# Performance work log

Hardware: AMD Instinct MI355X
Metric: run time of the kernel (lower is better)

The kernel has to match this reference:

```python
import jax, jax.numpy as jnp
import numpy as np

D_K = 64
EPS = 1e-6


def setup_inputs() -> dict:
    key = jax.random.key(0)
    ks = jax.random.split(key, 6)
    B, S, D2, DV = 4, 2048, 1024, 64
    q = jax.random.normal(ks[0], (B, S, D2), dtype=jnp.float32)
    k = jax.random.normal(ks[1], (B, S, D2), dtype=jnp.float32)
    v = jax.random.normal(ks[2], (B, S, D2), dtype=jnp.float32)
    mask = jax.random.randint(ks[3], (B, S, S), 0, 2) == 1
    V = jax.random.normal(ks[4], (1, DV), dtype=jnp.float32)
    fc_w = jax.random.normal(ks[5], (D2, DV), dtype=jnp.float32) * (1.0 / np.sqrt(DV))
    fc_b = jnp.zeros((D2,), dtype=jnp.float32)
    ln_g = jnp.ones((D2,), dtype=jnp.float32)
    ln_b = jnp.zeros((D2,), dtype=jnp.float32)
    return {"q": q, "k": k, "v": v, "mask": mask, "V": V,
            "fc_w": fc_w, "fc_b": fc_b, "ln_g": ln_g, "ln_b": ln_b}


def _layer_norm(x, g, b):
    mu = jnp.mean(x, axis=-1, keepdims=True)
    var = jnp.var(x, axis=-1, keepdims=True)
    return (x - mu) * jax.lax.rsqrt(var + EPS) * g + b


def reference(q, k, v, mask, V, fc_w, fc_b, ln_g, ln_b):
    residual = q
    qn = _layer_norm(q, ln_g, ln_b)
    # scaled dot-product scores (no softmax in this variant)
    attn = jnp.einsum('bsd,btd->bst', qn / jnp.sqrt(jnp.float32(D_K)), k)
    attn = jnp.where(mask, 0.0, attn)  # masked_fill with 0
    # v_ = V broadcast over (batch, seq, key); attn @ v_ == row-sum outer V
    output = jnp.sum(attn, axis=-1, keepdims=True) * V  # [B,S,d_v]
    output = output @ fc_w.T + fc_b                     # [B,S,2*d_model]
    output = output + residual
    return (output, attn)
```

## Files before the change

kernel.cpp:

```cpp
#include <hip/hip_runtime.h>
#include <hip/hip_bf16.h>
#include <cstdint>

#define S_LEN 2048
#define D2_   1024
#define DV_   64
#define NB_   4

typedef __bf16 bf16x8 __attribute__((ext_vector_type(8)));
typedef float  f32x4  __attribute__((ext_vector_type(4)));

__device__ __forceinline__ unsigned short f2bf(float f) {
  union { float f; unsigned int u; } v; v.f = f;
  unsigned int r = v.u + 0x7fffu + ((v.u >> 16) & 1u);
  return (unsigned short)(r >> 16);
}

__device__ __forceinline__ void async16(const unsigned short* g, unsigned short* l) {
  __builtin_amdgcn_global_load_lds(
      (__attribute__((address_space(1))) void*)g,
      (__attribute__((address_space(3))) void*)l,
      16, 0, 0);
}

__global__ void __launch_bounds__(256) prep_kernel(
    const float* __restrict__ q, const float* __restrict__ k,
    const float* __restrict__ gam, const float* __restrict__ bet,
    const float* __restrict__ V, const float* __restrict__ fw,
    unsigned short* __restrict__ qn, unsigned short* __restrict__ kb,
    float* __restrict__ w2) {
  const int row = blockIdx.x;
  const int t = threadIdx.x;

  const float4 x = ((const float4*)(q + (size_t)row * D2_))[t];
  float s  = x.x + x.y + x.z + x.w;
  float ss = x.x * x.x + x.y * x.y + x.z * x.z + x.w * x.w;
  #pragma unroll
  for (int o = 32; o > 0; o >>= 1) { s += __shfl_down(s, o); ss += __shfl_down(ss, o); }
  __shared__ float red[8];
  if ((t & 63) == 0) { red[t >> 6] = s; red[(t >> 6) + 4] = ss; }
  __syncthreads();
  const float tot  = red[0] + red[1] + red[2] + red[3];
  const float tots = red[4] + red[5] + red[6] + red[7];
  const float mu  = tot * (1.0f / D2_);
  const float var = tots * (1.0f / D2_) - mu * mu;
  const float rs  = rsqrtf(var + 1e-6f) * 0.125f;
  const float4 gv = ((const float4*)gam)[t];
  const float4 bv = ((const float4*)bet)[t];
  ushort4 o4;
  o4.x = f2bf((x.x - mu) * rs * gv.x + 0.125f * bv.x);
  o4.y = f2bf((x.y - mu) * rs * gv.y + 0.125f * bv.y);
  o4.z = f2bf((x.z - mu) * rs * gv.z + 0.125f * bv.z);
  o4.w = f2bf((x.w - mu) * rs * gv.w + 0.125f * bv.w);
  ((ushort4*)(qn + (size_t)row * D2_))[t] = o4;

  const float4 kx = ((const float4*)(k + (size_t)row * D2_))[t];
  ushort4 k4;
  k4.x = f2bf(kx.x); k4.y = f2bf(kx.y); k4.z = f2bf(kx.z); k4.w = f2bf(kx.w);
  ((ushort4*)(kb + (size_t)row * D2_))[t] = k4;

  if (row < 4) {
    const int d = row * 256 + t;
    const float4* r  = (const float4*)(fw + (size_t)d * DV_);
    const float4* vv = (const float4*)V;
    float acc = 0.f;
    #pragma unroll
    for (int j = 0; j < 16; ++j) {
      const float4 a = r[j], b = vv[j];
      acc += a.x * b.x + a.y * b.y + a.z * b.z + a.w * b.w;
    }
    w2[d] = acc;
  }
}

__global__ void __launch_bounds__(256) attn_gemm_kernel(
    const unsigned short* __restrict__ qn,
    const unsigned short* __restrict__ kb,
    const int* __restrict__ mask,
    float* __restrict__ attn) {
  __shared__ __align__(16) unsigned short Asm_[2][128 * 32];
  __shared__ __align__(16) unsigned short Bsm_[2][128 * 32];

  const int t  = threadIdx.x;
  const int bn = blockIdx.x * 128;
  const int bm = blockIdx.y * 128;
  const int bt = blockIdx.z;

  const unsigned short* gA = qn + ((size_t)bt * S_LEN + bm + (t >> 2)) * D2_ + (t & 3) * 8;
  const unsigned short* gB = kb + ((size_t)bt * S_LEN + bn + (t >> 2)) * D2_ + (t & 3) * 8;

  const int lane = t & 63;
  const int w  = t >> 6;
  const int wm = (w >> 1) * 64;
  const int wn = (w & 1) * 64;
  const int lr = lane & 15;
  const int lg = lane >> 4;

  f32x4 acc[4][4] = {};

  async16(gA, Asm_[0] + t * 8);
  async16(gA + 64 * D2_, Asm_[0] + t * 8 + 2048);
  async16(gB, Bsm_[0] + t * 8);
  async16(gB + 64 * D2_, Bsm_[0] + t * 8 + 2048);
  gA += 32; gB += 32;

  #pragma unroll 4
  for (int it = 0; it < 32; ++it) {
    __syncthreads();
    const unsigned short* Ac = Asm_[it & 1];
    const unsigned short* Bc = Bsm_[it & 1];
    if (it < 31) {
      unsigned short* An = Asm_[(it + 1) & 1];
      unsigned short* Bn = Bsm_[(it + 1) & 1];
      async16(gA, An + t * 8);
      async16(gA + 64 * D2_, An + t * 8 + 2048);
      async16(gB, Bn + t * 8);
      async16(gB + 64 * D2_, Bn + t * 8 + 2048);
      gA += 32; gB += 32;
    }
    bf16x8 af[4], bfv[4];
    #pragma unroll
    for (int f = 0; f < 4; ++f) {
      af[f]  = *(const bf16x8*)(Ac + (wm + f * 16 + lr) * 32 + lg * 8);
      bfv[f] = *(const bf16x8*)(Bc + (wn + f * 16 + lr) * 32 + lg * 8);
    }
    #pragma unroll
    for (int fm = 0; fm < 4; ++fm)
      #pragma unroll
      for (int fn = 0; fn < 4; ++fn)
        acc[fm][fn] = __builtin_amdgcn_mfma_f32_16x16x32_bf16(
            af[fm], bfv[fn], acc[fm][fn], 0, 0, 0);
  }

  #pragma unroll
  for (int fm = 0; fm < 4; ++fm) {
    #pragma unroll
    for (int r = 0; r < 4; ++r) {
      const int srow = bm + wm + fm * 16 + lg * 4 + r;
      const size_t off = ((size_t)bt * S_LEN + srow) * S_LEN + bn + wn;
      const int* mrow = mask + off;
      float*    arow = attn + off;
      #pragma unroll
      for (int fn = 0; fn < 4; ++fn) {
        const int c = fn * 16 + lr;
        float vv = acc[fm][fn][r];
        vv = mrow[c] ? 0.0f : vv;
        arow[c] = vv;
      }
    }
  }
}

__global__ void __launch_bounds__(256) out_kernel(
    const float* __restrict__ attn, const float* __restrict__ q,
    const float* __restrict__ w2, const float* __restrict__ fcb,
    float* __restrict__ out) {
  const int row = blockIdx.x;
  const int t = threadIdx.x;
  const float4* ar = (const float4*)(attn + (size_t)row * S_LEN);
  const float4 a = ar[t], b = ar[t + 256];
  float s = a.x + a.y + a.z + a.w + b.x + b.y + b.z + b.w;
  #pragma unroll
  for (int o = 32; o > 0; o >>= 1) s += __shfl_down(s, o);
  __shared__ float red[4];
  if ((t & 63) == 0) red[t >> 6] = s;
  __syncthreads();
  const float rs = red[0] + red[1] + red[2] + red[3];
  const float4 wv = ((const float4*)w2)[t];
  const float4 bv = ((const float4*)fcb)[t];
  const float4 qv = ((const float4*)(q + (size_t)row * D2_))[t];
  float4 o4;
  o4.x = rs * wv.x + bv.x + qv.x;
  o4.y = rs * wv.y + bv.y + qv.y;
  o4.z = rs * wv.z + bv.z + qv.z;
  o4.w = rs * wv.w + bv.w + qv.w;
  ((float4*)(out + (size_t)row * D2_))[t] = o4;
}

extern "C" void kernel_launch(void* const* d_in, const int* in_sizes, int n_in,
                              void* d_out, int out_size, void* d_ws, size_t ws_size,
                              hipStream_t stream) {
  (void)in_sizes; (void)n_in; (void)out_size; (void)ws_size;
  const float* q    = (const float*)d_in[0];
  const float* k    = (const float*)d_in[1];
  const int*   mask = (const int*)d_in[3];
  const float* V    = (const float*)d_in[4];
  const float* fw   = (const float*)d_in[5];
  const float* fcb  = (const float*)d_in[6];
  const float* lg   = (const float*)d_in[7];
  const float* lb   = (const float*)d_in[8];

  float* out  = (float*)d_out;
  float* attn = out + (size_t)NB_ * S_LEN * D2_;

  unsigned short* qn = (unsigned short*)out;
  unsigned short* kb = qn + (size_t)NB_ * S_LEN * D2_;
  float* w2 = (float*)d_ws;

  prep_kernel<<<NB_ * S_LEN, 256, 0, stream>>>(q, k, lg, lb, V, fw, qn, kb, w2);
  attn_gemm_kernel<<<dim3(S_LEN / 128, S_LEN / 128, NB_), 256, 0, stream>>>(qn, kb, mask, attn);
  out_kernel<<<NB_ * S_LEN, 256, 0, stream>>>(attn, q, w2, fcb, out);
}
```

Baseline: 295.6 us.

## Fuse row-sum into GEMM epilogue with atomics, switch to 32x32 MFMA and swizzled LDS

```diff
diff --git a/kernel.cpp b/kernel.cpp
--- a/kernel.cpp
+++ b/kernel.cpp
@@ -8,7 +8,7 @@
 #define NB_   4
 
 typedef __bf16 bf16x8 __attribute__((ext_vector_type(8)));
-typedef float  f32x4  __attribute__((ext_vector_type(4)));
+typedef float  f32x16 __attribute__((ext_vector_type(16)));
 
 __device__ __forceinline__ unsigned short f2bf(float f) {
   union { float f; unsigned int u; } v; v.f = f;
@@ -28,9 +28,11 @@
     const float* __restrict__ gam, const float* __restrict__ bet,
     const float* __restrict__ V, const float* __restrict__ fw,
     unsigned short* __restrict__ qn, unsigned short* __restrict__ kb,
-    float* __restrict__ w2) {
+    float* __restrict__ w2, float* __restrict__ rowsum) {
   const int row = blockIdx.x;
   const int t = threadIdx.x;
+
+  if (row < 32) rowsum[row * 256 + t] = 0.0f;
 
   const float4 x = ((const float4*)(q + (size_t)row * D2_))[t];
   float s  = x.x + x.y + x.z + x.w;
@@ -77,95 +79,91 @@
     const unsigned short* __restrict__ qn,
     const unsigned short* __restrict__ kb,
     const int* __restrict__ mask,
-    float* __restrict__ attn) {
-  __shared__ __align__(16) unsigned short Asm_[2][128 * 32];
-  __shared__ __align__(16) unsigned short Bsm_[2][128 * 32];
+    float* __restrict__ attn,
+    float* __restrict__ rowsum) {
+  __shared__ __align__(16) unsigned short Asm_[128 * 32];
+  __shared__ __align__(16) unsigned short Bsm_[128 * 32];
 
   const int t  = threadIdx.x;
   const int bn = blockIdx.x * 128;
   const int bm = blockIdx.y * 128;
   const int bt = blockIdx.z;
 
-  const unsigned short* gA = qn + ((size_t)bt * S_LEN + bm + (t >> 2)) * D2_ + (t & 3) * 8;
-  const unsigned short* gB = kb + ((size_t)bt * S_LEN + bn + (t >> 2)) * D2_ + (t & 3) * 8;
+  const int srow_ = t >> 2;
+  const int kg_   = (t & 3) ^ (srow_ & 3);
+  const unsigned short* gA = qn + ((size_t)bt * S_LEN + bm + srow_) * D2_ + kg_ * 8;
+  const unsigned short* gB = kb + ((size_t)bt * S_LEN + bn + srow_) * D2_ + kg_ * 8;
+  unsigned short* lA = Asm_ + t * 8;
+  unsigned short* lB = Bsm_ + t * 8;
 
   const int lane = t & 63;
-  const int w  = t >> 6;
-  const int wm = (w >> 1) * 64;
-  const int wn = (w & 1) * 64;
-  const int lr = lane & 15;
-  const int lg = lane >> 4;
-
-  f32x4 acc[4][4] = {};
-
-  async16(gA, Asm_[0] + t * 8);
-  async16(gA + 64 * D2_, Asm_[0] + t * 8 + 2048);
-  async16(gB, Bsm_[0] + t * 8);
-  async16(gB + 64 * D2_, Bsm_[0] + t * 8 + 2048);
-  gA += 32; gB += 32;
-
-  #pragma unroll 4
-  for (int it = 0; it < 32; ++it) {
+  const int w    = t >> 6;
+  const int wm   = (w >> 1) * 64;
+  const int wn   = (w & 1) * 64;
+  const int col  = lane & 31;
+  const int half = lane >> 5;
+
+  const int x0 = (half ^ (lane & 3)) * 8;
+  const int x1 = ((2 + half) ^ (lane & 3)) * 8;
+
+  f32x16 acc[2][2] = {};
+
+  for (int k0 = 0; k0 < D2_; k0 += 32) {
+    async16(gA, lA);
+    async16(gA + 64 * D2_, lA + 2048);
+    async16(gB, lB);
+    async16(gB + 64 * D2_, lB + 2048);
+    gA += 32; gB += 32;
     __syncthreads();
-    const unsigned short* Ac = Asm_[it & 1];
-    const unsigned short* Bc = Bsm_[it & 1];
-    if (it < 31) {
-      unsigned short* An = Asm_[(it + 1) & 1];
-      unsigned short* Bn = Bsm_[(it + 1) & 1];
-      async16(gA, An + t * 8);
-      async16(gA + 64 * D2_, An + t * 8 + 2048);
-      async16(gB, Bn + t * 8);
-      async16(gB + 64 * D2_, Bn + t * 8 + 2048);
-      gA += 32; gB += 32;
+
+    bf16x8 af[2][2], bfv[2][2];
+    #pragma unroll
+    for (int f = 0; f < 2; ++f) {
+      const int ra = (wm + f * 32 + col) * 32;
+      const int rb = (wn + f * 32 + col) * 32;
+      af[f][0]  = *(const bf16x8*)(Asm_ + ra + x0);
+      af[f][1]  = *(const bf16x8*)(Asm_ + ra + x1);
+      bfv[f][0] = *(const bf16x8*)(Bsm_ + rb + x0);
+      bfv[f][1] = *(const bf16x8*)(Bsm_ + rb + x1);
     }
-    bf16x8 af[4], bfv[4];
-    #pragma unroll
-    for (int f = 0; f < 4; ++f) {
-      af[f]  = *(const bf16x8*)(Ac + (wm + f * 16 + lr) * 32 + lg * 8);
-      bfv[f] = *(const bf16x8*)(Bc + (wn + f * 16 + lr) * 32 + lg * 8);
-    }
-    #pragma unroll
-    for (int fm = 0; fm < 4; ++fm)
+    #pragma unroll
+    for (int s = 0; s < 2; ++s)
       #pragma unroll
-      for (int fn = 0; fn < 4; ++fn)
-        acc[fm][fn] = __builtin_amdgcn_mfma_f32_16x16x32_bf16(
-            af[fm], bfv[fn], acc[fm][fn], 0, 0, 0);
+      for (int fm = 0; fm < 2; ++fm)
+        #pragma unroll
+        for (int fn = 0; fn < 2; ++fn)
+          acc[fm][fn] = __builtin_amdgcn_mfma_f32_32x32x16_bf16(
+              af[fm][s], bfv[fn][s], acc[fm][fn], 0, 0, 0);
+    __syncthreads();
   }
 
   #pragma unroll
-  for (int fm = 0; fm < 4; ++fm) {
-    #pragma unroll
-    for (int r = 0; r < 4; ++r) {
-      const int srow = bm + wm + fm * 16 + lg * 4 + r;
-      const size_t off = ((size_t)bt * S_LEN + srow) * S_LEN + bn + wn;
-      const int* mrow = mask + off;
-      float*    arow = attn + off;
+  for (int fm = 0; fm < 2; ++fm) {
+    #pragma unroll
+    for (int r = 0; r < 16; ++r) {
+      const int srow = bm + wm + fm * 32 + (r & 3) + 8 * (r >> 2) + 4 * half;
+      const size_t base = ((size_t)bt * S_LEN + srow) * S_LEN + bn + wn;
+      float v0 = acc[fm][0][r];
+      float v1 = acc[fm][1][r];
+      v0 = mask[base + col] ? 0.0f : v0;
+      v1 = mask[base + 32 + col] ? 0.0f : v1;
+      attn[base + col]      = v0;
+      attn[base + 32 + col] = v1;
+      float s = v0 + v1;
       #pragma unroll
-      for (int fn = 0; fn < 4; ++fn) {
-        const int c = fn * 16 + lr;
-        float vv = acc[fm][fn][r];
-        vv = mrow[c] ? 0.0f : vv;
-        arow[c] = vv;
-      }
+      for (int o = 16; o > 0; o >>= 1) s += __shfl_down(s, o, 32);
+      if (col == 0) atomicAdd(rowsum + (size_t)bt * S_LEN + srow, s);
     }
   }
 }
 
 __global__ void __launch_bounds__(256) out_kernel(
-    const float* __restrict__ attn, const float* __restrict__ q,
+    const float* __restrict__ rowsum, const float* __restrict__ q,
     const float* __restrict__ w2, const float* __restrict__ fcb,
     float* __restrict__ out) {
   const int row = blockIdx.x;
   const int t = threadIdx.x;
-  const float4* ar = (const float4*)(attn + (size_t)row * S_LEN);
-  const float4 a = ar[t], b = ar[t + 256];
-  float s = a.x + a.y + a.z + a.w + b.x + b.y + b.z + b.w;
-  #pragma unroll
-  for (int o = 32; o > 0; o >>= 1) s += __shfl_down(s, o);
-  __shared__ float red[4];
-  if ((t & 63) == 0) red[t >> 6] = s;
-  __syncthreads();
-  const float rs = red[0] + red[1] + red[2] + red[3];
+  const float rs = rowsum[row];
   const float4 wv = ((const float4*)w2)[t];
   const float4 bv = ((const float4*)fcb)[t];
   const float4 qv = ((const float4*)(q + (size_t)row * D2_))[t];
@@ -195,9 +193,10 @@
 
   unsigned short* qn = (unsigned short*)out;
   unsigned short* kb = qn + (size_t)NB_ * S_LEN * D2_;
-  float* w2 = (float*)d_ws;
-
-  prep_kernel<<<NB_ * S_LEN, 256, 0, stream>>>(q, k, lg, lb, V, fw, qn, kb, w2);
-  attn_gemm_kernel<<<dim3(S_LEN / 128, S_LEN / 128, NB_), 256, 0, stream>>>(qn, kb, mask, attn);
-  out_kernel<<<NB_ * S_LEN, 256, 0, stream>>>(attn, q, w2, fcb, out);
-}
+  float* w2     = (float*)d_ws;
+  float* rowsum = w2 + D2_;
+
+  prep_kernel<<<NB_ * S_LEN, 256, 0, stream>>>(q, k, lg, lb, V, fw, qn, kb, w2, rowsum);
+  attn_gemm_kernel<<<dim3(S_LEN / 128, S_LEN / 128, NB_), 256, 0, stream>>>(qn, kb, mask, attn, rowsum);
+  out_kernel<<<NB_ * S_LEN, 256, 0, stream>>>(rowsum, q, w2, fcb, out);
+}
```

Result: slower. 320.5 us (+8.4%).
